# Kernel optimization log

Measured on AMD Instinct MI355X. Metric: run time of the kernel, lower is better.

Reference implementation:

```python
import jax, jax.numpy as jnp
import numpy as np

DEPTH = 3  # chemprop default message passing depth


def setup_inputs() -> dict:
    key = jax.random.key(0)
    ks = jax.random.split(key, 10)
    n_atoms, n_bonds, max_nb, n_mols = 50000, 100000, 6, 2000
    atom_fdim, bond_fdim, hidden = 133, 147, 300
    f_atoms = jax.random.normal(ks[0], (n_atoms, atom_fdim), dtype=jnp.float32)
    f_bonds = jax.random.normal(ks[1], (n_bonds, bond_fdim), dtype=jnp.float32)
    a2b = jax.random.randint(ks[2], (n_atoms, max_nb), 0, n_bonds, dtype=jnp.int32)
    b2a = jax.random.randint(ks[3], (n_bonds,), 0, n_atoms, dtype=jnp.int32)
    b2revb = jax.random.randint(ks[4], (n_bonds,), 0, n_bonds, dtype=jnp.int32)
    mol_id = jnp.sort(jax.random.randint(ks[5], (n_atoms,), 0, n_mols, dtype=jnp.int32))
    W_i = jax.random.normal(ks[6], (bond_fdim, hidden), dtype=jnp.float32) * 0.05
    W_h = jax.random.normal(ks[7], (hidden, hidden), dtype=jnp.float32) * 0.05
    W_o = jax.random.normal(ks[8], (atom_fdim + hidden, hidden), dtype=jnp.float32) * 0.05
    b_o = jnp.zeros((hidden,), dtype=jnp.float32)
    return {"f_atoms": f_atoms, "f_bonds": f_bonds, "a2b": a2b, "b2a": b2a,
            "b2revb": b2revb, "mol_id": mol_id, "n_mols": n_mols,
            "W_i": W_i, "W_h": W_h, "W_o": W_o, "b_o": b_o}


def reference(f_atoms, f_bonds, a2b, b2a, b2revb, mol_id, n_mols, W_i, W_h, W_o, b_o):
    act = jax.nn.relu
    # W_i: bond features -> hidden; message init
    inp = f_bonds @ W_i                      # [n_bonds, h]
    message = act(inp)
    for _ in range(DEPTH - 1):
        nei = message[a2b]                    # [n_atoms, max_nb, h] gather
        a_message = nei.sum(axis=1)           # [n_atoms, h]
        rev = message[b2revb]                 # [n_bonds, h]
        message = a_message[b2a] - rev        # [n_bonds, h]
        message = act(inp + message @ W_h)
    # final atom readout
    a_message = message[a2b].sum(axis=1)      # [n_atoms, h]
    a_input = jnp.concatenate([f_atoms, a_message], axis=1)  # [n_atoms, fa+h]
    atom_hiddens = act(a_input @ W_o + b_o)   # [n_atoms, h]
    # ragged per-molecule mean (a_scope loop -> segment mean)
    sums = jax.ops.segment_sum(atom_hiddens, mol_id, num_segments=n_mols)
    counts = jax.ops.segment_sum(jnp.ones((atom_hiddens.shape[0],), dtype=atom_hiddens.dtype), mol_id, num_segments=n_mols)
    mol_vecs = jnp.where(counts[:, None] > 0, sums / jnp.maximum(counts, 1.0)[:, None], 0.0)
    return mol_vecs
```

## Files before the change

kernel.cpp:

```cpp
#include <hip/hip_runtime.h>
#include <cstddef>

#define H 300
#define RS 304
#define MAXNB 6
#define ASTR 312

typedef __attribute__((ext_vector_type(8)))  short bf16x8;
typedef __attribute__((ext_vector_type(16))) float f32x16;

__device__ __forceinline__ float bf2f(unsigned short u) {
    return __uint_as_float(((unsigned int)u) << 16);
}
__device__ __forceinline__ unsigned short f2bf(float f) {
    unsigned int u = __float_as_uint(f);
    u += 0x7FFFu + ((u >> 16) & 1u);
    return (unsigned short)(u >> 16);
}
__device__ __forceinline__ unsigned int sub2bf(unsigned int a, unsigned int b) {
    float d0 = bf2f((unsigned short)(a & 0xFFFFu)) - bf2f((unsigned short)(b & 0xFFFFu));
    float d1 = bf2f((unsigned short)(a >> 16))     - bf2f((unsigned short)(b >> 16));
    return (unsigned int)f2bf(d0) | ((unsigned int)f2bf(d1) << 16);
}
__device__ __forceinline__ unsigned int relu2(unsigned int w) {
    unsigned int r = w;
    if (w & 0x80000000u) r &= 0x0000FFFFu;
    if (w & 0x00008000u) r &= 0xFFFF0000u;
    return r;
}
__device__ __forceinline__ uint4 relu4(uint4 v) {
    v.x = relu2(v.x); v.y = relu2(v.y); v.z = relu2(v.z); v.w = relu2(v.w);
    return v;
}
__device__ __forceinline__ uint4 subpack4(uint4 a, uint4 b) {
    uint4 r;
    r.x = sub2bf(a.x, b.x); r.y = sub2bf(a.y, b.y);
    r.z = sub2bf(a.z, b.z); r.w = sub2bf(a.w, b.w);
    return r;
}


template<int S>
__global__ void __launch_bounds__(256)
pack_a_f32_c(const float* __restrict__ src, unsigned short* __restrict__ dst,
             int M, int K)
{
    __shared__ unsigned short sm[64 * 152];
    const int m0 = blockIdx.x * 64;
    const int r = threadIdx.x >> 2;
    const int q = threadIdx.x & 3;
    int mv = m0 + r; if (mv >= M) mv = M - 1;
    const float* rowF = src + (size_t)mv * K;
#pragma unroll
    for (int i = 0; i < (S * 4 + 3) / 4; ++i) {
        int c = q + i * 4;
        if (c * 4 < S * 16) {
            unsigned short h[4];
#pragma unroll
            for (int e = 0; e < 4; ++e) {
                int k = c * 4 + e;
                h[e] = (k < K) ? f2bf(rowF[k]) : (unsigned short)0;
            }
            uint2 o;
            o.x = (unsigned int)h[0] | ((unsigned int)h[1] << 16);
            o.y = (unsigned int)h[2] | ((unsigned int)h[3] << 16);
            *(uint2*)&sm[r * 152 + c * 4] = o;
        }
    }
    __syncthreads();
    for (int j = threadIdx.x; j < 2 * S * 64; j += 256) {
        int lane = j & 63;
        int t = j >> 6;
        int s = t % S;
        int mb2 = t / S;
        uint4 v = *(const uint4*)&sm[(mb2 * 32 + (lane & 31)) * 152 + s * 16 + (lane >> 5) * 8];
        int m_blk = blockIdx.x * 2 + mb2;
        *(uint4*)&dst[((size_t)(m_blk * S + s) * 64 + lane) * 8] = v;
    }
}

__global__ void __launch_bounds__(256)
pack_b(const float* __restrict__ src1, const float* __restrict__ src2,
       unsigned short* __restrict__ dst, int K1, int S1, int K2, int SB)
{
    int g = blockIdx.x * 256 + threadIdx.x;
    if (g >= 10 * SB * 64) return;
    int lane = g & 63;
    int t = g >> 6;
    int s = t % SB;
    int n_blk = t / SB;
    int n = n_blk * 32 + (lane & 31);
    unsigned int w[4];
#pragma unroll
    for (int p = 0; p < 4; ++p) {
        unsigned short h[2];
#pragma unroll
        for (int e = 0; e < 2; ++e) {
            int kf = s * 16 + (lane >> 5) * 8 + p * 2 + e;
            float v = 0.0f;
            if (n < H) {
                if (s < S1) {
                    if (kf < K1) v = src1[(size_t)kf * H + n];
                } else {
                    int k2 = kf - S1 * 16;
                    if (k2 < K2) v = src2[(size_t)k2 * H + n];
                }
            }
            h[e] = f2bf(v);
        }
        w[p] = (unsigned int)h[0] | ((unsigned int)h[1] << 16);
    }
    *(uint4*)&dst[(size_t)g * 8] = make_uint4(w[0], w[1], w[2], w[3]);
}

template<int RELU>
__global__ void __launch_bounds__(256)
aggregate_row(const unsigned short* __restrict__ msg, const int* __restrict__ a2b,
              unsigned short* __restrict__ amsg, int n_atoms)
{
    int gid = blockIdx.x * 256 + threadIdx.x;
    int total = n_atoms * 38;
    if (gid >= total) return;
    int atom = gid / 38;
    int g8 = gid - atom * 38;
    const int* nb = a2b + atom * MAXNB;
    float sum[8] = {};
#pragma unroll
    for (int j = 0; j < MAXNB; ++j) {
        int b = nb[j];
        uint4 v = *(const uint4*)&msg[(size_t)b * RS + g8 * 8];
        if (RELU) v = relu4(v);
        unsigned int ww[4] = {v.x, v.y, v.z, v.w};
#pragma unroll
        for (int p = 0; p < 4; ++p) {
            sum[p * 2]     += bf2f((unsigned short)(ww[p] & 0xFFFFu));
            sum[p * 2 + 1] += bf2f((unsigned short)(ww[p] >> 16));
        }
    }
    unsigned int ow[4];
#pragma unroll
    for (int p = 0; p < 4; ++p)
        ow[p] = (unsigned int)f2bf(sum[p * 2]) | ((unsigned int)f2bf(sum[p * 2 + 1]) << 16);
    *(uint4*)&amsg[(size_t)atom * RS + g8 * 8] = make_uint4(ow[0], ow[1], ow[2], ow[3]);
}

template<int S1, int S2, int SBL, int MODE, int RELUMSG>
__global__ void __launch_bounds__(256)
gemm_fused(const unsigned short* __restrict__ A1,
           const unsigned short* __restrict__ amsg,
           const unsigned short* __restrict__ msg,
           const int* __restrict__ b2a, const int* __restrict__ b2revb,
           const unsigned short* __restrict__ Bp,
           const float* __restrict__ bias,
           const unsigned short* __restrict__ inp_add,
           const float* __restrict__ Adense, int Kd,
           unsigned short* __restrict__ out, int M)
{
    __shared__ __align__(16) unsigned short smem[64 * ASTR];

    const int lane  = threadIdx.x & 63;
    const int w     = threadIdx.x >> 6;
    const int rbase = (w >> 1) * 32;
    const int cbase = (w & 1) * 160;
    const int mrow  = lane & 31;
    const int quad  = lane >> 5;
    const int m0    = blockIdx.x * 64;
    const int m_blk = blockIdx.x * 2 + (w >> 1);
    const int nblk0 = cbase >> 5;

    {
        const int r = threadIdx.x >> 2;
        const int q = threadIdx.x & 3;
        int mm = m0 + r;
        int mv = (mm < M) ? mm : 0;
        if (MODE == 0) {
            if (mm >= M) mv = M - 1;
            const float* rowF = Adense + (size_t)mv * Kd;
#pragma unroll
            for (int i = 0; i < (S2 * 4 + 3) / 4; ++i) {
                int c = q + i * 4;
                if (c * 4 < S2 * 16) {
                    unsigned short h[4];
#pragma unroll
                    for (int e = 0; e < 4; ++e) {
                        int k = c * 4 + e;
                        h[e] = (k < Kd) ? f2bf(rowF[k]) : (unsigned short)0;
                    }
                    uint2 o;
                    o.x = (unsigned int)h[0] | ((unsigned int)h[1] << 16);
                    o.y = (unsigned int)h[2] | ((unsigned int)h[3] << 16);
                    *(uint2*)&smem[r * ASTR + c * 4] = o;
                }
            }
            __syncthreads();
        } else if (MODE == 1 || MODE == 2) {
            const unsigned short* rowA;
            const unsigned short* rowM = nullptr;
            if (MODE == 1) {
                rowA = amsg + (size_t)b2a[mv] * RS;
                rowM = msg  + (size_t)b2revb[mv] * RS;
            } else {
                rowA = amsg + (size_t)mv * RS;
            }
#pragma unroll
            for (int i = 0; i < 10; ++i) {
                int c = q + i * 4;
                if (c < 38) {
                    uint4 o;
                    if (MODE == 1) {
                        uint4 va = *(const uint4*)(rowA + c * 8);
                        uint4 vm = *(const uint4*)(rowM + c * 8);
                        if (RELUMSG) vm = relu4(vm);
                        o = subpack4(va, vm);
                    } else {
                        o = *(const uint4*)(rowA + c * 8);
                    }
                    *(uint4*)&smem[r * ASTR + c * 8] = o;
                }
            }
            __syncthreads();
        }
    }

    f32x16 acc[5];
#pragma unroll
    for (int t = 0; t < 5; ++t)
#pragma unroll
        for (int i = 0; i < 16; ++i) acc[t][i] = 0.0f;

    const unsigned short* pa1 = (S1 > 0) ? (A1 + ((size_t)m_blk * S1 * 64 + lane) * 8) : nullptr;
    const unsigned short* pb  = Bp + ((size_t)nblk0 * SBL * 64 + lane) * 8;

    constexpr int STOT = S1 + S2;

    auto loadA = [&](int s) -> bf16x8 {
        if (s < S1) return *(const bf16x8*)(pa1 + (size_t)s * 512);
        return *(const bf16x8*)&smem[(rbase + mrow) * ASTR + (s - S1) * 16 + quad * 8];
    };

    bf16x8 b0[5], b1[5];
#pragma unroll
    for (int nt = 0; nt < 5; ++nt) b0[nt] = *(const bf16x8*)(pb + ((size_t)nt * SBL + 0) * 512);
    if (STOT > 1) {
#pragma unroll
        for (int nt = 0; nt < 5; ++nt) b1[nt] = *(const bf16x8*)(pb + ((size_t)nt * SBL + 1) * 512);
    }

#pragma unroll
    for (int s = 0; s < STOT; s += 2) {
        bf16x8 a = loadA(s);
        acc[0] = __builtin_amdgcn_mfma_f32_32x32x16_bf16(a, b0[0], acc[0], 0, 0, 0);
        acc[1] = __builtin_amdgcn_mfma_f32_32x32x16_bf16(a, b0[1], acc[1], 0, 0, 0);
        acc[2] = __builtin_amdgcn_mfma_f32_32x32x16_bf16(a, b0[2], acc[2], 0, 0, 0);
        acc[3] = __builtin_amdgcn_mfma_f32_32x32x16_bf16(a, b0[3], acc[3], 0, 0, 0);
        acc[4] = __builtin_amdgcn_mfma_f32_32x32x16_bf16(a, b0[4], acc[4], 0, 0, 0);
        if (s + 2 < STOT) {
#pragma unroll
            for (int nt = 0; nt < 5; ++nt) b0[nt] = *(const bf16x8*)(pb + ((size_t)nt * SBL + s + 2) * 512);
        }
        if (s + 1 < STOT) {
            bf16x8 a2 = loadA(s + 1);
            acc[0] = __builtin_amdgcn_mfma_f32_32x32x16_bf16(a2, b1[0], acc[0], 0, 0, 0);
            acc[1] = __builtin_amdgcn_mfma_f32_32x32x16_bf16(a2, b1[1], acc[1], 0, 0, 0);
            acc[2] = __builtin_amdgcn_mfma_f32_32x32x16_bf16(a2, b1[2], acc[2], 0, 0, 0);
            acc[3] = __builtin_amdgcn_mfma_f32_32x32x16_bf16(a2, b1[3], acc[3], 0, 0, 0);
            acc[4] = __builtin_amdgcn_mfma_f32_32x32x16_bf16(a2, b1[4], acc[4], 0, 0, 0);
            if (s + 3 < STOT) {
#pragma unroll
                for (int nt = 0; nt < 5; ++nt) b1[nt] = *(const bf16x8*)(pb + ((size_t)nt * SBL + s + 3) * 512);
            }
        }
    }

    __syncthreads();

#pragma unroll
    for (int nt = 0; nt < 5; ++nt) {
        int col = cbase + nt * 32 + mrow;
#pragma unroll
        for (int r = 0; r < 16; ++r) {
            int row = rbase + (r & 3) + 8 * (r >> 2) + 4 * quad;
            if (col < 308) smem[row * 308 + col] = f2bf(acc[nt][r]);
        }
    }
    __syncthreads();

    for (int idx = threadIdx.x; idx < 64 * 76; idx += 256) {
        int row = idx / 76, gcol = idx - row * 76;
        int mm = m0 + row;
        if (mm >= M) continue;
        int c0 = gcol * 4;
        uint2 raw = *(const uint2*)&smem[row * 308 + c0];
        uint2 o;
        if (MODE == 0) {
            o = raw;
        } else {
            unsigned short h[4] = {(unsigned short)(raw.x & 0xFFFFu), (unsigned short)(raw.x >> 16),
                                   (unsigned short)(raw.y & 0xFFFFu), (unsigned short)(raw.y >> 16)};
            float v[4];
#pragma unroll
            for (int e = 0; e < 4; ++e) v[e] = bf2f(h[e]);
            if (MODE == 1) {
                uint2 iv = *(const uint2*)&inp_add[(size_t)mm * RS + c0];
                v[0] += bf2f((unsigned short)(iv.x & 0xFFFFu));
                v[1] += bf2f((unsigned short)(iv.x >> 16));
                v[2] += bf2f((unsigned short)(iv.y & 0xFFFFu));
                v[3] += bf2f((unsigned short)(iv.y >> 16));
            } else {
#pragma unroll
                for (int e = 0; e < 4; ++e) v[e] += (c0 + e < H) ? bias[c0 + e] : 0.0f;
            }
#pragma unroll
            for (int e = 0; e < 4; ++e) h[e] = f2bf(fmaxf(v[e], 0.0f));
            o.x = (unsigned int)h[0] | ((unsigned int)h[1] << 16);
            o.y = (unsigned int)h[2] | ((unsigned int)h[3] << 16);
        }
        *(uint2*)&out[(size_t)mm * RS + c0] = o;
    }
}

__global__ void __launch_bounds__(128)
segmean_kernel(const unsigned short* __restrict__ ah,
               const int* __restrict__ mol_id, int n_atoms,
               float* __restrict__ out)
{
    int m = blockIdx.x;
    int lo = 0, hi = n_atoms;
    while (lo < hi) { int mid = (lo + hi) >> 1; if (mol_id[mid] < m) lo = mid + 1; else hi = mid; }
    int start = lo;
    hi = n_atoms;
    while (lo < hi) { int mid = (lo + hi) >> 1; if (mol_id[mid] < m + 1) lo = mid + 1; else hi = mid; }
    int end = lo;

    int c = threadIdx.x;
    float a0 = 0.f, a1 = 0.f, a2 = 0.f;
    for (int a = start; a < end; ++a) {
        const unsigned short* row = ah + (size_t)a * RS;
        a0 += bf2f(row[c]);
        a1 += bf2f(row[c + 128]);
        if (c < H - 256) a2 += bf2f(row[c + 256]);
    }
    float inv = (end > start) ? 1.0f / (float)(end - start) : 0.0f;
    float* orow = out + (size_t)m * H;
    orow[c] = a0 * inv;
    orow[c + 128] = a1 * inv;
    if (c < H - 256) orow[c + 256] = a2 * inv;
}

extern "C" void kernel_launch(void* const* d_in, const int* in_sizes, int n_in,
                              void* d_out, int out_size, void* d_ws, size_t ws_size,
                              hipStream_t stream)
{
    const float* f_atoms = (const float*)d_in[0];
    const float* f_bonds = (const float*)d_in[1];
    const int*   a2b     = (const int*)d_in[2];
    const int*   b2a     = (const int*)d_in[3];
    const int*   b2revb  = (const int*)d_in[4];
    const int*   mol_id  = (const int*)d_in[5];
    const float* W_i     = (const float*)d_in[7];
    const float* W_h     = (const float*)d_in[8];
    const float* W_o     = (const float*)d_in[9];
    const float* b_o     = (const float*)d_in[10];

    const int n_atoms   = in_sizes[5];
    const int n_bonds   = in_sizes[3];
    const int atom_fdim = in_sizes[0] / n_atoms;
    const int bond_fdim = in_sizes[1] / n_bonds;
    const int n_mols    = out_size / H;

    const int gBonds = (n_bonds + 63) / 64;
    const int gAtoms = (n_atoms + 63) / 64;
    const int MBa = 2 * gAtoms;

    const size_t bondsRS = (size_t)n_bonds * RS;
    const size_t atomsRS = (size_t)n_atoms * RS;
    const size_t fapSz   = (size_t)MBa * 9 * 512;
    const size_t wihSz   = 10 * 30 * 512;
    const size_t woSz    = 10 * 29 * 512;
    const size_t wh19Sz  = 10 * 19 * 512;

    unsigned short* inp  = (unsigned short*)d_ws;
    unsigned short* msgB = inp  + bondsRS;
    unsigned short* amsg = msgB + bondsRS;
    unsigned short* wih  = amsg + atomsRS;
    unsigned short* wo   = wih  + wihSz;
    unsigned short* wh19 = wo   + woSz;
    unsigned short* ah   = wh19 + wh19Sz;
    unsigned short* fap  = inp;

    dim3 blk(256);
    const int aggBlocks = (n_atoms * 38 + 255) / 256;

    pack_b<<<(10 * 30 * 64 + 255) / 256, blk, 0, stream>>>(W_i, W_h, wih, bond_fdim, 10, H, 30);
    pack_b<<<(10 * 19 * 64 + 255) / 256, blk, 0, stream>>>(W_h, W_h, wh19, H, 19, 0, 19);
    pack_b<<<(10 * 29 * 64 + 255) / 256, blk, 0, stream>>>(W_o, W_o + (size_t)atom_fdim * H, wo,
                                                           atom_fdim, 9, H, 29);

    gemm_fused<0, 10, 30, 0, 0><<<gBonds, blk, 0, stream>>>(
        nullptr, nullptr, nullptr, nullptr, nullptr, wih, nullptr, nullptr,
        f_bonds, bond_fdim, inp, n_bonds);

    aggregate_row<1><<<aggBlocks, blk, 0, stream>>>(inp, a2b, amsg, n_atoms);
    gemm_fused<0, 19, 19, 1, 1><<<gBonds, blk, 0, stream>>>(
        nullptr, amsg, inp, b2a, b2revb, wh19, nullptr, inp, nullptr, 0, msgB, n_bonds);

    aggregate_row<0><<<aggBlocks, blk, 0, stream>>>(msgB, a2b, amsg, n_atoms);
    gemm_fused<0, 19, 19, 1, 0><<<gBonds, blk, 0, stream>>>(
        nullptr, amsg, msgB, b2a, b2revb, wh19, nullptr, inp, nullptr, 0, inp, n_bonds);

    aggregate_row<0><<<aggBlocks, blk, 0, stream>>>(inp, a2b, amsg, n_atoms);

    pack_a_f32_c<9><<<gAtoms, blk, 0, stream>>>(f_atoms, fap, n_atoms, atom_fdim);

    gemm_fused<9, 19, 29, 2, 0><<<gAtoms, blk, 0, stream>>>(
        fap, amsg, nullptr, nullptr, nullptr, wo, b_o, nullptr, nullptr, 0, ah, n_atoms);

    segmean_kernel<<<n_mols, dim3(128), 0, stream>>>(ah, mol_id, n_atoms, (float*)d_out);
}
```

Measured before the change: 516.3 us.

## Make fused GEMM persistent with double-buffered LDS prefetch of next tile

Converts gemm_fused into a persistent kernel with a capped grid that loops over 64-row tiles. The gathered A rows for the next tile are loaded into registers during the current tile's epilogue and written into a second LDS buffer, so global-load latency overlaps with the MFMA work and the output writes. The cost is twice the shared memory, more live registers (fa[40], va/vm arrays) that may cause spills even with launch_bounds(256,2), and hardcoded grid caps of 512 and 392.

Result: slower. 1.122 ms (+117.2%).

```diff
diff --git a/kernel.cpp b/kernel.cpp
--- a/kernel.cpp
+++ b/kernel.cpp
@@ -38,6 +38,12 @@
     r.z = sub2bf(a.z, b.z); r.w = sub2bf(a.w, b.w);
     return r;
 }
+
+#define BARRIER_NOVM() do { \
+    asm volatile("s_waitcnt lgkmcnt(0)" ::: "memory"); \
+    __builtin_amdgcn_s_barrier(); \
+    asm volatile("" ::: "memory"); \
+} while (0)
 
 
 template<int S>
@@ -145,7 +151,7 @@
 }
 
 template<int S1, int S2, int SBL, int MODE, int RELUMSG>
-__global__ void __launch_bounds__(256)
+__global__ void __launch_bounds__(256, 2)
 gemm_fused(const unsigned short* __restrict__ A1,
            const unsigned short* __restrict__ amsg,
            const unsigned short* __restrict__ msg,
@@ -156,7 +162,7 @@
            const float* __restrict__ Adense, int Kd,
            unsigned short* __restrict__ out, int M)
 {
-    __shared__ __align__(16) unsigned short smem[64 * ASTR];
+    __shared__ __align__(16) unsigned short smem[2][64 * ASTR];
 
     const int lane  = threadIdx.x & 63;
     const int w     = threadIdx.x >> 6;
@@ -164,158 +170,230 @@
     const int cbase = (w & 1) * 160;
     const int mrow  = lane & 31;
     const int quad  = lane >> 5;
-    const int m0    = blockIdx.x * 64;
-    const int m_blk = blockIdx.x * 2 + (w >> 1);
     const int nblk0 = cbase >> 5;
-
-    {
-        const int r = threadIdx.x >> 2;
-        const int q = threadIdx.x & 3;
-        int mm = m0 + r;
-        int mv = (mm < M) ? mm : 0;
+    const int r     = threadIdx.x >> 2;
+    const int q     = threadIdx.x & 3;
+
+    const int ntiles = (M + 63) >> 6;
+    const int G = gridDim.x;
+
+    const unsigned short* pb = Bp + ((size_t)nblk0 * SBL * 64 + lane) * 8;
+    constexpr int STOT = S1 + S2;
+
+    float fa[40];
+    uint4 va[10];
+    uint4 vm[10];
+    int idxA = 0, idxB = 0;
+
+    auto load_idx = [&](int t) {
+        if (MODE == 1) {
+            int mm = t * 64 + r;
+            int mv = (mm < M) ? mm : 0;
+            idxA = b2a[mv];
+            idxB = b2revb[mv];
+        }
+    };
+
+    auto stage_issue = [&](int t) {
+        int mm = t * 64 + r;
         if (MODE == 0) {
-            if (mm >= M) mv = M - 1;
+            int mv = (mm < M) ? mm : (M - 1);
             const float* rowF = Adense + (size_t)mv * Kd;
 #pragma unroll
-            for (int i = 0; i < (S2 * 4 + 3) / 4; ++i) {
-                int c = q + i * 4;
-                if (c * 4 < S2 * 16) {
-                    unsigned short h[4];
-#pragma unroll
-                    for (int e = 0; e < 4; ++e) {
-                        int k = c * 4 + e;
-                        h[e] = (k < Kd) ? f2bf(rowF[k]) : (unsigned short)0;
-                    }
-                    uint2 o;
-                    o.x = (unsigned int)h[0] | ((unsigned int)h[1] << 16);
-                    o.y = (unsigned int)h[2] | ((unsigned int)h[3] << 16);
-                    *(uint2*)&smem[r * ASTR + c * 4] = o;
-                }
-            }
-            __syncthreads();
-        } else if (MODE == 1 || MODE == 2) {
-            const unsigned short* rowA;
-            const unsigned short* rowM = nullptr;
-            if (MODE == 1) {
-                rowA = amsg + (size_t)b2a[mv] * RS;
-                rowM = msg  + (size_t)b2revb[mv] * RS;
+            for (int i = 0; i < 10; ++i) {
+                int c = q + i * 4;
+#pragma unroll
+                for (int e = 0; e < 4; ++e) {
+                    int k = c * 4 + e;
+                    fa[i * 4 + e] = (k < Kd) ? rowF[k] : 0.0f;
+                }
+            }
+        } else if (MODE == 1) {
+            const unsigned short* rowA = amsg + (size_t)idxA * RS;
+            const unsigned short* rowM = msg  + (size_t)idxB * RS;
+#pragma unroll
+            for (int i = 0; i < 10; ++i) {
+                int c = q + i * 4;
+                if (c < 38) {
+                    va[i] = *(const uint4*)(rowA + c * 8);
+                    vm[i] = *(const uint4*)(rowM + c * 8);
+                }
+            }
+        } else {
+            int mv = (mm < M) ? mm : 0;
+            const unsigned short* rowA = amsg + (size_t)mv * RS;
+#pragma unroll
+            for (int i = 0; i < 10; ++i) {
+                int c = q + i * 4;
+                if (c < 38) va[i] = *(const uint4*)(rowA + c * 8);
+            }
+        }
+    };
+
+    auto stage_commit = [&](int pp) {
+        unsigned short* dst = smem[pp];
+        if (MODE == 0) {
+#pragma unroll
+            for (int i = 0; i < 10; ++i) {
+                int c = q + i * 4;
+                unsigned short h0 = f2bf(fa[i * 4 + 0]);
+                unsigned short h1 = f2bf(fa[i * 4 + 1]);
+                unsigned short h2 = f2bf(fa[i * 4 + 2]);
+                unsigned short h3 = f2bf(fa[i * 4 + 3]);
+                uint2 o;
+                o.x = (unsigned int)h0 | ((unsigned int)h1 << 16);
+                o.y = (unsigned int)h2 | ((unsigned int)h3 << 16);
+                *(uint2*)&dst[r * ASTR + c * 4] = o;
+            }
+        } else if (MODE == 1) {
+#pragma unroll
+            for (int i = 0; i < 10; ++i) {
+                int c = q + i * 4;
+                if (c < 38) {
+                    uint4 m4 = RELUMSG ? relu4(vm[i]) : vm[i];
+                    *(uint4*)&dst[r * ASTR + c * 8] = subpack4(va[i], m4);
+                }
+            }
+        } else {
+#pragma unroll
+            for (int i = 0; i < 10; ++i) {
+                int c = q + i * 4;
+                if (c < 38) *(uint4*)&dst[r * ASTR + c * 8] = va[i];
+            }
+        }
+    };
+
+    f32x16 acc[5];
+    bf16x8 b0[5], b1[5];
+
+    int tile = blockIdx.x;
+    load_idx(tile);
+    stage_issue(tile);
+    load_idx(tile + G);
+    stage_commit(0);
+#pragma unroll
+    for (int nt = 0; nt < 5; ++nt)
+        b0[nt] = *(const bf16x8*)(pb + ((size_t)nt * SBL) * 512);
+#pragma unroll
+    for (int t = 0; t < 5; ++t)
+#pragma unroll
+        for (int i = 0; i < 16; ++i) acc[t][i] = 0.0f;
+    BARRIER_NOVM();
+
+    int p = 0;
+    while (true) {
+        const unsigned short* As = smem[p];
+        const unsigned short* pa1 = (S1 > 0)
+            ? (A1 + ((size_t)(tile * 2 + (w >> 1)) * S1 * 64 + lane) * 8)
+            : (const unsigned short*)nullptr;
+
+        if (STOT > 1) {
+#pragma unroll
+            for (int nt = 0; nt < 5; ++nt)
+                b1[nt] = *(const bf16x8*)(pb + ((size_t)nt * SBL + 1) * 512);
+        }
+
+        auto loadA = [&](int s) -> bf16x8 {
+            if (s < S1) return *(const bf16x8*)(pa1 + (size_t)s * 512);
+            return *(const bf16x8*)&As[(rbase + mrow) * ASTR + (s - S1) * 16 + quad * 8];
+        };
+
+#pragma unroll
+        for (int s = 0; s < STOT; s += 2) {
+            bf16x8 a = loadA(s);
+            acc[0] = __builtin_amdgcn_mfma_f32_32x32x16_bf16(a, b0[0], acc[0], 0, 0, 0);
+            acc[1] = __builtin_amdgcn_mfma_f32_32x32x16_bf16(a, b0[1], acc[1], 0, 0, 0);
+            acc[2] = __builtin_amdgcn_mfma_f32_32x32x16_bf16(a, b0[2], acc[2], 0, 0, 0);
+            acc[3] = __builtin_amdgcn_mfma_f32_32x32x16_bf16(a, b0[3], acc[3], 0, 0, 0);
+            acc[4] = __builtin_amdgcn_mfma_f32_32x32x16_bf16(a, b0[4], acc[4], 0, 0, 0);
+            if (s + 2 < STOT) {
+#pragma unroll
+                for (int nt = 0; nt < 5; ++nt)
+                    b0[nt] = *(const bf16x8*)(pb + ((size_t)nt * SBL + s + 2) * 512);
+            }
+            if (s + 1 < STOT) {
+                bf16x8 a2 = loadA(s + 1);
+                acc[0] = __builtin_amdgcn_mfma_f32_32x32x16_bf16(a2, b1[0], acc[0], 0, 0, 0);
+                acc[1] = __builtin_amdgcn_mfma_f32_32x32x16_bf16(a2, b1[1], acc[1], 0, 0, 0);
+                acc[2] = __builtin_amdgcn_mfma_f32_32x32x16_bf16(a2, b1[2], acc[2], 0, 0, 0);
+                acc[3] = __builtin_amdgcn_mfma_f32_32x32x16_bf16(a2, b1[3], acc[3], 0, 0, 0);
+                acc[4] = __builtin_amdgcn_mfma_f32_32x32x16_bf16(a2, b1[4], acc[4], 0, 0, 0);
+                if (s + 3 < STOT) {
+#pragma unroll
+                    for (int nt = 0; nt < 5; ++nt)
+                        b1[nt] = *(const bf16x8*)(pb + ((size_t)nt * SBL + s + 3) * 512);
+                }
+            }
+        }
+
+        const int ntile = tile + G;
+        const bool hasNext = (ntile < ntiles);
+        if (hasNext) {
+            stage_issue(ntile);
+            load_idx(ntile + G);
+#pragma unroll
+            for (int nt = 0; nt < 5; ++nt)
+                b0[nt] = *(const bf16x8*)(pb + ((size_t)nt * SBL) * 512);
+        }
+
+        BARRIER_NOVM();
+
+        unsigned short* Cs = smem[p];
+#pragma unroll
+        for (int nt = 0; nt < 5; ++nt) {
+            int col = cbase + nt * 32 + mrow;
+#pragma unroll
+            for (int rr = 0; rr < 16; ++rr) {
+                int row = rbase + (rr & 3) + 8 * (rr >> 2) + 4 * quad;
+                if (col < 308) Cs[row * 308 + col] = f2bf(acc[nt][rr]);
+            }
+        }
+        BARRIER_NOVM();
+
+        const int m0 = tile * 64;
+        for (int idx = threadIdx.x; idx < 64 * 76; idx += 256) {
+            int row = idx / 76, gcol = idx - row * 76;
+            int mm = m0 + row;
+            if (mm >= M) continue;
+            int c0 = gcol * 4;
+            uint2 raw = *(const uint2*)&Cs[row * 308 + c0];
+            uint2 o;
+            if (MODE == 0) {
+                o = raw;
             } else {
-                rowA = amsg + (size_t)mv * RS;
-            }
-#pragma unroll
-            for (int i = 0; i < 10; ++i) {
-                int c = q + i * 4;
-                if (c < 38) {
-                    uint4 o;
-                    if (MODE == 1) {
-                        uint4 va = *(const uint4*)(rowA + c * 8);
-                        uint4 vm = *(const uint4*)(rowM + c * 8);
-                        if (RELUMSG) vm = relu4(vm);
-                        o = subpack4(va, vm);
-                    } else {
-                        o = *(const uint4*)(rowA + c * 8);
-                    }
-                    *(uint4*)&smem[r * ASTR + c * 8] = o;
-                }
-            }
-            __syncthreads();
-        }
-    }
-
-    f32x16 acc[5];
-#pragma unroll
-    for (int t = 0; t < 5; ++t)
-#pragma unroll
-        for (int i = 0; i < 16; ++i) acc[t][i] = 0.0f;
-
-    const unsigned short* pa1 = (S1 > 0) ? (A1 + ((size_t)m_blk * S1 * 64 + lane) * 8) : nullptr;
-    const unsigned short* pb  = Bp + ((size_t)nblk0 * SBL * 64 + lane) * 8;
-
-    constexpr int STOT = S1 + S2;
-
-    auto loadA = [&](int s) -> bf16x8 {
-        if (s < S1) return *(const bf16x8*)(pa1 + (size_t)s * 512);
-        return *(const bf16x8*)&smem[(rbase + mrow) * ASTR + (s - S1) * 16 + quad * 8];
-    };
-
-    bf16x8 b0[5], b1[5];
-#pragma unroll
-    for (int nt = 0; nt < 5; ++nt) b0[nt] = *(const bf16x8*)(pb + ((size_t)nt * SBL + 0) * 512);
-    if (STOT > 1) {
-#pragma unroll
-        for (int nt = 0; nt < 5; ++nt) b1[nt] = *(const bf16x8*)(pb + ((size_t)nt * SBL + 1) * 512);
-    }
-
-#pragma unroll
-    for (int s = 0; s < STOT; s += 2) {
-        bf16x8 a = loadA(s);
-        acc[0] = __builtin_amdgcn_mfma_f32_32x32x16_bf16(a, b0[0], acc[0], 0, 0, 0);
-        acc[1] = __builtin_amdgcn_mfma_f32_32x32x16_bf16(a, b0[1], acc[1], 0, 0, 0);
-        acc[2] = __builtin_amdgcn_mfma_f32_32x32x16_bf16(a, b0[2], acc[2], 0, 0, 0);
-        acc[3] = __builtin_amdgcn_mfma_f32_32x32x16_bf16(a, b0[3], acc[3], 0, 0, 0);
-        acc[4] = __builtin_amdgcn_mfma_f32_32x32x16_bf16(a, b0[4], acc[4], 0, 0, 0);
-        if (s + 2 < STOT) {
-#pragma unroll
-            for (int nt = 0; nt < 5; ++nt) b0[nt] = *(const bf16x8*)(pb + ((size_t)nt * SBL + s + 2) * 512);
-        }
-        if (s + 1 < STOT) {
-            bf16x8 a2 = loadA(s + 1);
-            acc[0] = __builtin_amdgcn_mfma_f32_32x32x16_bf16(a2, b1[0], acc[0], 0, 0, 0);
-            acc[1] = __builtin_amdgcn_mfma_f32_32x32x16_bf16(a2, b1[1], acc[1], 0, 0, 0);
-            acc[2] = __builtin_amdgcn_mfma_f32_32x32x16_bf16(a2, b1[2], acc[2], 0, 0, 0);
-            acc[3] = __builtin_amdgcn_mfma_f32_32x32x16_bf16(a2, b1[3], acc[3], 0, 0, 0);
-            acc[4] = __builtin_amdgcn_mfma_f32_32x32x16_bf16(a2, b1[4], acc[4], 0, 0, 0);
-            if (s + 3 < STOT) {
-#pragma unroll
-                for (int nt = 0; nt < 5; ++nt) b1[nt] = *(const bf16x8*)(pb + ((size_t)nt * SBL + s + 3) * 512);
-            }
-        }
-    }
-
-    __syncthreads();
-
-#pragma unroll
-    for (int nt = 0; nt < 5; ++nt) {
-        int col = cbase + nt * 32 + mrow;
-#pragma unroll
-        for (int r = 0; r < 16; ++r) {
-            int row = rbase + (r & 3) + 8 * (r >> 2) + 4 * quad;
-            if (col < 308) smem[row * 308 + col] = f2bf(acc[nt][r]);
-        }
-    }
-    __syncthreads();
-
-    for (int idx = threadIdx.x; idx < 64 * 76; idx += 256) {
-        int row = idx / 76, gcol = idx - row * 76;
-        int mm = m0 + row;
-        if (mm >= M) continue;
-        int c0 = gcol * 4;
-        uint2 raw = *(const uint2*)&smem[row * 308 + c0];
-        uint2 o;
-        if (MODE == 0) {
-            o = raw;
-        } else {
-            unsigned short h[4] = {(unsigned short)(raw.x & 0xFFFFu), (unsigned short)(raw.x >> 16),
-                                   (unsigned short)(raw.y & 0xFFFFu), (unsigned short)(raw.y >> 16)};
-            float v[4];
-#pragma unroll
-            for (int e = 0; e < 4; ++e) v[e] = bf2f(h[e]);
-            if (MODE == 1) {
-                uint2 iv = *(const uint2*)&inp_add[(size_t)mm * RS + c0];
-                v[0] += bf2f((unsigned short)(iv.x & 0xFFFFu));
-                v[1] += bf2f((unsigned short)(iv.x >> 16));
-                v[2] += bf2f((unsigned short)(iv.y & 0xFFFFu));
-                v[3] += bf2f((unsigned short)(iv.y >> 16));
-            } else {
-#pragma unroll
-                for (int e = 0; e < 4; ++e) v[e] += (c0 + e < H) ? bias[c0 + e] : 0.0f;
-            }
-#pragma unroll
-            for (int e = 0; e < 4; ++e) h[e] = f2bf(fmaxf(v[e], 0.0f));
-            o.x = (unsigned int)h[0] | ((unsigned int)h[1] << 16);
-            o.y = (unsigned int)h[2] | ((unsigned int)h[3] << 16);
-        }
-        *(uint2*)&out[(size_t)mm * RS + c0] = o;
+                unsigned short h[4] = {(unsigned short)(raw.x & 0xFFFFu), (unsigned short)(raw.x >> 16),
+                                       (unsigned short)(raw.y & 0xFFFFu), (unsigned short)(raw.y >> 16)};
+                float v[4];
+#pragma unroll
+                for (int e = 0; e < 4; ++e) v[e] = bf2f(h[e]);
+                if (MODE == 1) {
+                    uint2 iv = *(const uint2*)&inp_add[(size_t)mm * RS + c0];
+                    v[0] += bf2f((unsigned short)(iv.x & 0xFFFFu));
+                    v[1] += bf2f((unsigned short)(iv.x >> 16));
+                    v[2] += bf2f((unsigned short)(iv.y & 0xFFFFu));
+                    v[3] += bf2f((unsigned short)(iv.y >> 16));
+                } else {
+#pragma unroll
+                    for (int e = 0; e < 4; ++e) v[e] += (c0 + e < H) ? bias[c0 + e] : 0.0f;
+                }
+#pragma unroll
+                for (int e = 0; e < 4; ++e) h[e] = f2bf(fmaxf(v[e], 0.0f));
+                o.x = (unsigned int)h[0] | ((unsigned int)h[1] << 16);
+                o.y = (unsigned int)h[2] | ((unsigned int)h[3] << 16);
+            }
+            *(uint2*)&out[(size_t)mm * RS + c0] = o;
+        }
+
+        if (!hasNext) break;
+
+        stage_commit(p ^ 1);
+#pragma unroll
+        for (int t = 0; t < 5; ++t)
+#pragma unroll
+            for (int i = 0; i < 16; ++i) acc[t][i] = 0.0f;
+        BARRIER_NOVM();
+        p ^= 1;
+        tile = ntile;
     }
 }
 
@@ -368,13 +446,14 @@
     const int bond_fdim = in_sizes[1] / n_bonds;
     const int n_mols    = out_size / H;
 
-    const int gBonds = (n_bonds + 63) / 64;
     const int gAtoms = (n_atoms + 63) / 64;
-    const int MBa = 2 * gAtoms;
+    const int tilesB = (n_bonds + 63) / 64;
+    const int tilesA = gAtoms;
+    const int gridB = (tilesB < 512) ? tilesB : 512;
+    const int gridA = (tilesA < 392) ? tilesA : 392;
 
     const size_t bondsRS = (size_t)n_bonds * RS;
     const size_t atomsRS = (size_t)n_atoms * RS;
-    const size_t fapSz   = (size_t)MBa * 9 * 512;
     const size_t wihSz   = 10 * 30 * 512;
     const size_t woSz    = 10 * 29 * 512;
     const size_t wh19Sz  = 10 * 19 * 512;
@@ -396,23 +475,23 @@
     pack_b<<<(10 * 29 * 64 + 255) / 256, blk, 0, stream>>>(W_o, W_o + (size_t)atom_fdim * H, wo,
                                                            atom_fdim, 9, H, 29);
 
-    gemm_fused<0, 10, 30, 0, 0><<<gBonds, blk, 0, stream>>>(
+    gemm_fused<0, 10, 30, 0, 0><<<gridB, blk, 0, stream>>>(
         nullptr, nullptr, nullptr, nullptr, nullptr, wih, nullptr, nullptr,
         f_bonds, bond_fdim, inp, n_bonds);
 
     aggregate_row<1><<<aggBlocks, blk, 0, stream>>>(inp, a2b, amsg, n_atoms);
-    gemm_fused<0, 19, 19, 1, 1><<<gBonds, blk, 0, stream>>>(
+    gemm_fused<0, 19, 19, 1, 1><<<gridB, blk, 0, stream>>>(
         nullptr, amsg, inp, b2a, b2revb, wh19, nullptr, inp, nullptr, 0, msgB, n_bonds);
 
     aggregate_row<0><<<aggBlocks, blk, 0, stream>>>(msgB, a2b, amsg, n_atoms);
-    gemm_fused<0, 19, 19, 1, 0><<<gBonds, blk, 0, stream>>>(
+    gemm_fused<0, 19, 19, 1, 0><<<gridB, blk, 0, stream>>>(
         nullptr, amsg, msgB, b2a, b2revb, wh19, nullptr, inp, nullptr, 0, inp, n_bonds);
 
     aggregate_row<0><<<aggBlocks, blk, 0, stream>>>(inp, a2b, amsg, n_atoms);
 
     pack_a_f32_c<9><<<gAtoms, blk, 0, stream>>>(f_atoms, fap, n_atoms, atom_fdim);
 
-    gemm_fused<9, 19, 29, 2, 0><<<gAtoms, blk, 0, stream>>>(
+    gemm_fused<9, 19, 29, 2, 0><<<gridA, blk, 0, stream>>>(
         fap, amsg, nullptr, nullptr, nullptr, wo, b_o, nullptr, nullptr, 0, ah, n_atoms);
 
     segmean_kernel<<<n_mols, dim3(128), 0, stream>>>(ah, mol_id, n_atoms, (float*)d_out);
```
